# Kernel optimization log

Measured on AMD Instinct MI355X. Metric: run time of the kernel, lower is better.

## Reference

```python
import jax, jax.numpy as jnp
import numpy as np

DELTA = 1e-08
P = 3
Q = 3
M = 128   # ctrl pts in u
N = 128   # ctrl pts in v
OUT_U = 1024
OUT_V = 1024
DIM = 3
BATCH = 4


def gen_knot_vector(p, n_ctrl):
    # clamped uniform knot vector, length n_ctrl + p + 1 (NURBSDiff convention)
    return np.concatenate([np.zeros(p), np.linspace(0.0, 1.0, n_ctrl - p + 1), np.ones(p)]).astype(np.float64)


def find_span(n_ctrl, p, u, U):
    # NURBS book A2.1
    n = n_ctrl - 1
    if u >= U[n + 1]:
        return n
    if u <= U[p]:
        return p
    low, high = p, n + 1
    mid = (low + high) // 2
    while u < U[mid] or u >= U[mid + 1]:
        if u < U[mid]:
            high = mid
        else:
            low = mid
        mid = (low + high) // 2
    return mid


def basis_funs(i, u, p, U):
    # NURBS book A2.2 (Cox-de Boor)
    Nf = np.zeros(p + 1)
    Nf[0] = 1.0
    left = np.zeros(p + 1)
    right = np.zeros(p + 1)
    for j in range(1, p + 1):
        left[j] = u - U[i + 1 - j]
        right[j] = U[i + j] - u
        saved = 0.0
        for r in range(j):
            temp = Nf[r] / (right[r + 1] + left[j - r])
            Nf[r] = saved + right[r + 1] * temp
            saved = left[j - r] * temp
        Nf[j] = saved
    return Nf


def precompute(p, n_ctrl, out_dim):
    U = gen_knot_vector(p, n_ctrl)
    params = np.linspace(0.0 + DELTA, 1.0 - DELTA, out_dim)
    spans = np.empty(out_dim, dtype=np.int32)
    basis = np.empty((out_dim, p + 1), dtype=np.float32)
    for k, u in enumerate(params):
        s = find_span(n_ctrl, p, u, U)
        spans[k] = s
        basis[k] = basis_funs(s, u, p, U)
    return spans, basis


def setup_inputs() -> dict:
    key = jax.random.key(0)
    uspan, Nu = precompute(P, M, OUT_U)
    vspan, Nv = precompute(Q, N, OUT_V)
    ctrl_pts = jax.random.normal(key, (BATCH, M, N, DIM + 1), dtype=jnp.float32)
    # keep homogeneous weight channel positive & away from 0 to avoid divide blowup
    ctrl_pts = ctrl_pts.at[..., DIM].set(1.0 + 0.1 * jax.nn.sigmoid(ctrl_pts[..., DIM]))
    return {
        "ctrl_pts": ctrl_pts,
        "Nu": jnp.asarray(Nu),            # [OUT_U, P+1]
        "Nv": jnp.asarray(Nv),            # [OUT_V, Q+1]
        "uspan": jnp.asarray(uspan),      # [OUT_U] int32
        "vspan": jnp.asarray(vspan),      # [OUT_V] int32
    }


def reference(ctrl_pts, Nu, Nv, uspan, vspan):
    p = Nu.shape[1] - 1
    q = Nv.shape[1] - 1
    # local control-point index windows
    uidx = uspan[:, None] - p + jnp.arange(p + 1)  # [U, p+1]
    vidx = vspan[:, None] - q + jnp.arange(q + 1)  # [V, q+1]
    # gather along u and contract with u-basis: [B,U,p+1,n,D] -> [B,U,n,D]
    gu = ctrl_pts[:, uidx]                         # [B, U, p+1, n, D]
    tu = jnp.einsum('ul,bulnd->bund', Nu, gu)      # [B, U, n, D]
    # gather along v and contract with v-basis: [B,U,V,q+1,D] -> [B,U,V,D]
    gv = tu[:, :, vidx]                            # [B, U, V, q+1, D]
    sw = jnp.einsum('vr,buvrd->buvd', Nv, gv)      # [B, U, V, D] homogeneous
    return sw[..., :DIM] / sw[..., DIM:DIM + 1]
```

## Files before the change

kernel.cpp:

```cpp
#include <hip/hip_runtime.h>


#define OUT_U 1024
#define OUT_V 1024
#define MCTRL 128
#define NCTRL 128

typedef float f4 __attribute__((ext_vector_type(4)));
typedef float vfloat3 __attribute__((ext_vector_type(3), aligned(4)));

__global__ __launch_bounds__(256) void surf_eval_kernel(
    const f4*  __restrict__ ctrl,
    const f4*  __restrict__ Nu,
    const f4*  __restrict__ Nv,
    const int* __restrict__ uspan,
    const int* __restrict__ vspan,
    float*     __restrict__ out)
{
    __shared__ f4 tu[4][NCTRL];

    const int tid  = threadIdx.x;
    const int w    = tid >> 6;
    const int lane = tid & 63;
    const int u    = blockIdx.x >> 1;
    const int half = blockIdx.x & 1;

    const int us = uspan[u];
    const f4  nu = Nu[u];

    const f4* win = ctrl + ((size_t)(w * MCTRL + (us - 3)) * NCTRL);
#pragma unroll
    for (int h = 0; h < 2; ++h) {
        const int j = lane + h * 64;
        f4 acc = nu.x * win[j];
        acc += nu.y * win[NCTRL + j];
        acc += nu.z * win[2 * NCTRL + j];
        acc += nu.w * win[3 * NCTRL + j];
        tu[w][j] = acc;
    }

    const size_t outrow = ((size_t)w * OUT_U + (size_t)u) * OUT_V;
    const int    vbase  = (half << 9) + lane;
#pragma unroll 4
    for (int k = 0; k < 8; ++k) {
        const int v  = vbase + (k << 6);
        const int vs = vspan[v];
        const f4  nv = Nv[v];

        const f4 t0 = tu[w][vs - 3];
        const f4 t1 = tu[w][vs - 2];
        const f4 t2 = tu[w][vs - 1];
        const f4 t3 = tu[w][vs];

        f4 acc = nv.x * t0;
        acc += nv.y * t1;
        acc += nv.z * t2;
        acc += nv.w * t3;

        const float inv = __builtin_amdgcn_rcpf(acc.w);
        vfloat3 res;
        res.x = acc.x * inv;
        res.y = acc.y * inv;
        res.z = acc.z * inv;
        __builtin_nontemporal_store(res, (vfloat3*)(out + (outrow + (size_t)v) * 3));
    }
}

extern "C" void kernel_launch(void* const* d_in, const int* in_sizes, int n_in,
                              void* d_out, int out_size, void* d_ws, size_t ws_size,
                              hipStream_t stream) {
    const f4*  ctrl  = (const f4*)d_in[0];
    const f4*  Nu    = (const f4*)d_in[1];
    const f4*  Nv    = (const f4*)d_in[2];
    const int* uspan = (const int*)d_in[3];
    const int* vspan = (const int*)d_in[4];
    float*     out   = (float*)d_out;

    const int nblocks = OUT_U * 2;
    surf_eval_kernel<<<nblocks, 256, 0, stream>>>(ctrl, Nu, Nv, uspan, vspan, out);
}
```

Before: 15.98 us.

## Process four consecutive v points per thread with shared 5-point window and 16B stores

Each thread now evaluates four consecutive v samples, loading spans as an int4, reading a shared five-entry window of the u-contracted row from LDS, and shifting the basis weights when the span increments within the group. The three results per point are packed into three 16-byte nontemporal stores instead of per-point 12-byte stores. This cuts LDS reads and makes global writes wider and aligned. It relies on spans changing by at most one within four consecutive samples, which holds for this grid density.

```diff
diff --git a/kernel.cpp b/kernel.cpp
--- a/kernel.cpp
+++ b/kernel.cpp
@@ -7,7 +7,6 @@
 #define NCTRL 128
 
 typedef float f4 __attribute__((ext_vector_type(4)));
-typedef float vfloat3 __attribute__((ext_vector_type(3), aligned(4)));
 
 __global__ __launch_bounds__(256) void surf_eval_kernel(
     const f4*  __restrict__ ctrl,
@@ -40,29 +39,52 @@
     }
 
     const size_t outrow = ((size_t)w * OUT_U + (size_t)u) * OUT_V;
-    const int    vbase  = (half << 9) + lane;
-#pragma unroll 4
-    for (int k = 0; k < 8; ++k) {
-        const int v  = vbase + (k << 6);
-        const int vs = vspan[v];
-        const f4  nv = Nv[v];
+#pragma unroll
+    for (int k = 0; k < 2; ++k) {
+        const int v0 = (half << 9) + (k << 8) + (lane << 2);
+        const int4 vs4 = *(const int4*)(vspan + v0);
+        const int m  = vs4.x;
+        const int wb = m - 3;
 
-        const f4 t0 = tu[w][vs - 3];
-        const f4 t1 = tu[w][vs - 2];
-        const f4 t2 = tu[w][vs - 1];
-        const f4 t3 = tu[w][vs];
+        f4 W0 = tu[w][wb];
+        f4 W1 = tu[w][wb + 1];
+        f4 W2 = tu[w][wb + 2];
+        f4 W3 = tu[w][wb + 3];
+        f4 W4 = tu[w][min(wb + 4, NCTRL - 1)];
 
-        f4 acc = nv.x * t0;
-        acc += nv.y * t1;
-        acc += nv.z * t2;
-        acc += nv.w * t3;
+        float r[12];
+#pragma unroll
+        for (int p = 0; p < 4; ++p) {
+            const int vsp = (p == 0) ? vs4.x : (p == 1) ? vs4.y
+                          : (p == 2) ? vs4.z : vs4.w;
+            const bool c = (vsp != m);
+            const f4 nv = Nv[v0 + p];
 
-        const float inv = __builtin_amdgcn_rcpf(acc.w);
-        vfloat3 res;
-        res.x = acc.x * inv;
-        res.y = acc.y * inv;
-        res.z = acc.z * inv;
-        __builtin_nontemporal_store(res, (vfloat3*)(out + (outrow + (size_t)v) * 3));
+            const float w0 = c ? 0.0f : nv.x;
+            const float w1 = c ? nv.x : nv.y;
+            const float w2 = c ? nv.y : nv.z;
+            const float w3 = c ? nv.z : nv.w;
+            const float w4 = c ? nv.w : 0.0f;
+
+            f4 acc = w0 * W0;
+            acc += w1 * W1;
+            acc += w2 * W2;
+            acc += w3 * W3;
+            acc += w4 * W4;
+
+            const float inv = __builtin_amdgcn_rcpf(acc.w);
+            r[p * 3 + 0] = acc.x * inv;
+            r[p * 3 + 1] = acc.y * inv;
+            r[p * 3 + 2] = acc.z * inv;
+        }
+
+        f4* op = (f4*)(out + (outrow + (size_t)v0) * 3);
+        f4 s0 = {r[0], r[1], r[2],  r[3]};
+        f4 s1 = {r[4], r[5], r[6],  r[7]};
+        f4 s2 = {r[8], r[9], r[10], r[11]};
+        __builtin_nontemporal_store(s0, op);
+        __builtin_nontemporal_store(s1, op + 1);
+        __builtin_nontemporal_store(s2, op + 2);
     }
 }
 
```

Result: slower. 26.45 us (+65.6%).
